# Kernel optimization log

Hardware: AMD Instinct MI355X
Metric: run time of the kernel (lower is better)

## Reference

```python
import jax, jax.numpy as jnp
import numpy as np

N, E, B, T = 50000, 800000, 256, 50
IN_DIM, H, C1, C2, Q_DIM, LH = 128, 4, 32, 128, 32, 128
EPS = 1e-5


def setup_inputs() -> dict:
    key = jax.random.key(0)
    ks = jax.random.split(key, 24)
    g = 0.05
    inp = {
        'x': jax.random.normal(ks[0], (N, IN_DIM), jnp.float32),
        'edge_index': jax.random.randint(ks[1], (2, E), 0, N, jnp.int32),
        'batch': jnp.sort(jax.random.randint(ks[2], (N,), 0, B, jnp.int32)),
        'quant': jax.random.normal(ks[3], (B, T, Q_DIM), jnp.float32),
        # GATConv(128 -> 32, heads=4, concat)
        'gat_W': jax.random.normal(ks[4], (IN_DIM, H * C1), jnp.float32) * g,
        'gat_att_src': jax.random.normal(ks[5], (H, C1), jnp.float32) * g,
        'gat_att_dst': jax.random.normal(ks[6], (H, C1), jnp.float32) * g,
        'gat_b': jnp.zeros((H * C1,), jnp.float32),
        # BN1 over 128 channels (eval mode)
        'bn1_gamma': jnp.ones((H * C1,), jnp.float32),
        'bn1_beta': jnp.zeros((H * C1,), jnp.float32),
        'bn1_mean': jax.random.normal(ks[7], (H * C1,), jnp.float32) * 0.01,
        'bn1_var': jnp.ones((H * C1,), jnp.float32),
        # GCNConv(128 -> 128)
        'gcn_W': jax.random.normal(ks[8], (H * C1, C2), jnp.float32) * g,
        'gcn_b': jnp.zeros((C2,), jnp.float32),
        'bn2_gamma': jnp.ones((C2,), jnp.float32),
        'bn2_beta': jnp.zeros((C2,), jnp.float32),
        'bn2_mean': jax.random.normal(ks[9], (C2,), jnp.float32) * 0.01,
        'bn2_var': jnp.ones((C2,), jnp.float32),
        # GlobalAttention gate: Linear(C2 -> 1)
        'gate_W': jax.random.normal(ks[10], (1, C2), jnp.float32) * g,
        'gate_b': jnp.zeros((1,), jnp.float32),
        # LSTM(Q_DIM -> LH), torch gate order i,f,g,o
        'lstm_Wih': jax.random.normal(ks[11], (4 * LH, Q_DIM), jnp.float32) * g,
        'lstm_Whh': jax.random.normal(ks[12], (4 * LH, LH), jnp.float32) * g,
        'lstm_bih': jnp.zeros((4 * LH,), jnp.float32),
        'lstm_bhh': jnp.zeros((4 * LH,), jnp.float32),
        # final Linear(C2+LH -> 1)
        'fc_W': jax.random.normal(ks[13], (1, C2 + LH), jnp.float32) * g,
        'fc_b': jnp.zeros((1,), jnp.float32),
    }
    return inp


def _segment_softmax(e, seg, num_segments):
    m = jax.ops.segment_max(e, seg, num_segments=num_segments)
    ex = jnp.exp(e - m[seg])
    s = jax.ops.segment_sum(ex, seg, num_segments=num_segments)
    return ex / (s[seg] + 1e-16)


def _bn_eval(x, gamma, beta, mean, var):
    return gamma * (x - mean) * jax.lax.rsqrt(var + EPS) + beta


def _forward(x, edge_index, batch, quant,
             gat_W, gat_att_src, gat_att_dst, gat_b,
             bn1_gamma, bn1_beta, bn1_mean, bn1_var,
             gcn_W, gcn_b, bn2_gamma, bn2_beta, bn2_mean, bn2_var,
             gate_W, gate_b,
             lstm_Wih, lstm_Whh, lstm_bih, lstm_bhh,
             fc_W, fc_b):
    n = x.shape[0]
    loops = jnp.arange(n, dtype=edge_index.dtype)
    ei = jnp.concatenate([edge_index, jnp.stack([loops, loops])], axis=1)  # add self loops
    src, dst = ei[0], ei[1]

    # ---- GATConv ----
    xw = (x @ gat_W).reshape(n, H, C1)                      # [N,H,C1]
    a_src = jnp.sum(xw * gat_att_src, axis=-1)              # [N,H]
    a_dst = jnp.sum(xw * gat_att_dst, axis=-1)
    e = jax.nn.leaky_relu(a_src[src] + a_dst[dst], 0.2)     # [E+N,H]
    alpha = _segment_softmax(e, dst, n)                     # softmax over in-edges per dst
    msg = xw[src] * alpha[:, :, None]                       # [E+N,H,C1]
    h = jax.ops.segment_sum(msg, dst, num_segments=n).reshape(n, H * C1) + gat_b

    h = jax.nn.elu(h)
    h = _bn_eval(h, bn1_gamma, bn1_beta, bn1_mean, bn1_var)

    # ---- GCNConv (sym-normalized with self loops) ----
    deg = jax.ops.segment_sum(jnp.ones_like(dst, jnp.float32), dst, num_segments=n)
    dinv = jnp.where(deg > 0, jax.lax.rsqrt(deg), 0.0)
    norm = dinv[src] * dinv[dst]                            # [E+N]
    hw = h @ gcn_W                                          # [N,C2]
    h2 = jax.ops.segment_sum(hw[src] * norm[:, None], dst, num_segments=n) + gcn_b

    h2 = jax.nn.elu(h2)
    h2 = _bn_eval(h2, bn2_gamma, bn2_beta, bn2_mean, bn2_var)

    # ---- GlobalAttention pooling over graphs ----
    gate = (h2 @ gate_W.T + gate_b)[:, 0]                   # [N]
    score = _segment_softmax(gate, batch, B)
    graph_rep = jax.ops.segment_sum(score[:, None] * h2, batch, num_segments=B)  # [B,C2]

    # ---- LSTM over quant series ----
    def step(carry, xt):
        hh, cc = carry
        gates = xt @ lstm_Wih.T + hh @ lstm_Whh.T + lstm_bih + lstm_bhh
        i, f, gg, o = jnp.split(gates, 4, axis=-1)
        cc = jax.nn.sigmoid(f) * cc + jax.nn.sigmoid(i) * jnp.tanh(gg)
        hh = jax.nn.sigmoid(o) * jnp.tanh(cc)
        return (hh, cc), None

    h0 = jnp.zeros((B, LH), quant.dtype)
    (hT, _), _ = jax.lax.scan(step, (h0, h0), jnp.swapaxes(quant, 0, 1))

    combined = jnp.concatenate([graph_rep, hT], axis=1)     # [B, C2+LH]
    out = (combined @ fc_W.T + fc_b)[:, 0]                  # [B]
    return out


def reference(x, edge_index, batch, quant,
              gat_W, gat_att_src, gat_att_dst, gat_b,
              bn1_gamma, bn1_beta, bn1_mean, bn1_var,
              gcn_W, gcn_b, bn2_gamma, bn2_beta, bn2_mean, bn2_var,
              gate_W, gate_b,
              lstm_Wih, lstm_Whh, lstm_bih, lstm_bhh,
              fc_W, fc_b):
    return _forward(x, edge_index, batch, quant,
                    gat_W, gat_att_src, gat_att_dst, gat_b,
                    bn1_gamma, bn1_beta, bn1_mean, bn1_var,
                    gcn_W, gcn_b, bn2_gamma, bn2_beta, bn2_mean, bn2_var,
                    gate_W, gate_b,
                    lstm_Wih, lstm_Whh, lstm_bih, lstm_bhh,
                    fc_W, fc_b)
```

## Files before the change

kernel.cpp:

```cpp
#include <hip/hip_runtime.h>
#include <cfloat>
#include <cstddef>

constexpr int KIN   = 128;
constexpr int KQD   = 32;
constexpr int KT    = 50;
constexpr int KLH   = 128;
constexpr float BN_EPS = 1e-5f;

typedef __attribute__((ext_vector_type(8))) short bf16x8;
typedef __attribute__((ext_vector_type(4))) float f32x4;
union U8 { bf16x8 v; unsigned u[4]; };

__device__ __forceinline__ float elu_f(float x)  { return x > 0.f ? x : (__expf(x) - 1.f); }
__device__ __forceinline__ float leaky_f(float x){ return x > 0.f ? x : 0.2f * x; }

__device__ __forceinline__ unsigned bfpack(float lo, float hi) {
    unsigned ul = __float_as_uint(lo), uh = __float_as_uint(hi);
    ul += 0x7FFFu + ((ul >> 16) & 1u);
    uh += 0x7FFFu + ((uh >> 16) & 1u);
    return (ul >> 16) | (uh & 0xFFFF0000u);
}
__device__ __forceinline__ unsigned short bf1(float v) {
    unsigned u = __float_as_uint(v);
    u += 0x7FFFu + ((u >> 16) & 1u);
    return (unsigned short)(u >> 16);
}
__device__ __forceinline__ float bflo(unsigned u) { return __uint_as_float(u << 16); }
__device__ __forceinline__ float bfhi(unsigned u) { return __uint_as_float(u & 0xFFFF0000u); }

__device__ __forceinline__ bf16x8 pack8(float4 p, float4 q) {
    U8 t;
    t.u[0] = bfpack(p.x, p.y); t.u[1] = bfpack(p.z, p.w);
    t.u[2] = bfpack(q.x, q.y); t.u[3] = bfpack(q.z, q.w);
    return t.v;
}

__global__ void k_deg(const int* __restrict__ ei, int E, int* __restrict__ deg) {
    int e = blockIdx.x * blockDim.x + threadIdx.x;
    if (e < E) atomicAdd(&deg[ei[E + e]], 1);
}

__global__ __launch_bounds__(1024)
void k_scan_a(const int* __restrict__ deg, int n, int* __restrict__ bsum) {
    __shared__ int wsum[16];
    int tid = threadIdx.x, lane = tid & 63, w = tid >> 6;
    int i0 = blockIdx.x * 4096 + tid * 4;
    int t = 0;
    #pragma unroll
    for (int j = 0; j < 4; j++) t += (i0 + j < n) ? deg[i0 + j] : 0;
    #pragma unroll
    for (int d = 1; d < 64; d <<= 1) t += __shfl_xor(t, d);
    if (lane == 0) wsum[w] = t;
    __syncthreads();
    if (tid == 0) {
        int s = 0;
        #pragma unroll
        for (int k = 0; k < 16; k++) s += wsum[k];
        bsum[blockIdx.x] = s;
    }
}

__global__ void k_scan_b(int* __restrict__ bsum, int nb) {
    if (threadIdx.x == 0) {
        int run = 0;
        for (int i = 0; i < nb; i++) { int v = bsum[i]; bsum[i] = run; run += v; }
    }
}

__global__ __launch_bounds__(1024)
void k_scan_c(const int* __restrict__ deg, int n, const int* __restrict__ bsum,
              int* __restrict__ offsets, int* __restrict__ cursor,
              float* __restrict__ dinv) {
    __shared__ int wsum[16];
    int tid = threadIdx.x, lane = tid & 63, w = tid >> 6;
    int i0 = blockIdx.x * 4096 + tid * 4;
    int v[4];
    #pragma unroll
    for (int j = 0; j < 4; j++) v[j] = (i0 + j < n) ? deg[i0 + j] : 0;
    int tsum = v[0] + v[1] + v[2] + v[3];
    int sc = tsum;
    #pragma unroll
    for (int d = 1; d < 64; d <<= 1) {
        int o = __shfl_up(sc, d);
        if (lane >= d) sc += o;
    }
    if (lane == 63) wsum[w] = sc;
    __syncthreads();
    if (w == 0) {
        int xx = (lane < 16) ? wsum[lane] : 0;
        #pragma unroll
        for (int d = 1; d < 16; d <<= 1) {
            int o = __shfl_up(xx, d);
            if (lane >= d) xx += o;
        }
        if (lane < 16) wsum[lane] = xx;
    }
    __syncthreads();
    int run = bsum[blockIdx.x] + ((w > 0) ? wsum[w - 1] : 0) + sc - tsum;
    #pragma unroll
    for (int j = 0; j < 4; j++) {
        int i = i0 + j;
        if (i < n) {
            cursor[i]      = run;
            offsets[i + 1] = run + v[j];
            dinv[i]        = rsqrtf((float)(v[j] + 1));
            run += v[j];
        }
    }
    if (blockIdx.x == 0 && tid == 0) offsets[0] = 0;
}

__global__ void k_fill(const int* __restrict__ ei, int E, int* __restrict__ cursor,
                       int* __restrict__ csr_src) {
    int e = blockIdx.x * blockDim.x + threadIdx.x;
    if (e < E) {
        int s = ei[e], d = ei[E + e];
        int pos = atomicAdd(&cursor[d], 1);
        csr_src[pos] = s;
    }
}

template <bool ATT>
__global__ __launch_bounds__(256, 4)
void k_gemm_mfma(const float* __restrict__ X, const float* __restrict__ W,
                 unsigned* __restrict__ Yb, int nrows,
                 const float* __restrict__ attS, const float* __restrict__ attD,
                 float* __restrict__ a_src, float* __restrict__ a_dst) {
    __shared__ float tile[16][132];
    __shared__ float as_sh[128], ad_sh[128];
    int tid  = threadIdx.x;
    int lane = tid & 63;
    int wv   = tid >> 6;
    if (ATT && tid < 128) { as_sh[tid] = attS[tid]; ad_sh[tid] = attD[tid]; }
    int l16 = lane & 15;
    int kq  = (lane >> 4) * 8;
    bf16x8 bfr[2][4];
    #pragma unroll
    for (int nt = 0; nt < 2; nt++) {
        int n = wv * 32 + nt * 16 + l16;
        #pragma unroll
        for (int kk = 0; kk < 4; kk++) {
            int k0 = kk * 32 + kq;
            float f[8];
            #pragma unroll
            for (int j = 0; j < 8; j++) f[j] = W[(size_t)(k0 + j) * 128 + n];
            U8 t;
            t.u[0] = bfpack(f[0], f[1]); t.u[1] = bfpack(f[2], f[3]);
            t.u[2] = bfpack(f[4], f[5]); t.u[3] = bfpack(f[6], f[7]);
            bfr[nt][kk] = t.v;
        }
    }
    int nch = (nrows + 15) / 16;
    for (int ch = blockIdx.x; ch < nch; ch += gridDim.x) {
        int r0 = ch * 16;
        int r  = r0 + l16;
        bool rok = r < nrows;
        const float* xr = X + (size_t)r * 128 + kq;
        float4 z4 = make_float4(0.f, 0.f, 0.f, 0.f);
        bf16x8 afr[4];
        #pragma unroll
        for (int kk = 0; kk < 4; kk++) {
            float4 p = rok ? *reinterpret_cast<const float4*>(xr + kk * 32)     : z4;
            float4 q = rok ? *reinterpret_cast<const float4*>(xr + kk * 32 + 4) : z4;
            afr[kk] = pack8(p, q);
        }
        f32x4 acc0 = {0.f, 0.f, 0.f, 0.f};
        f32x4 acc1 = {0.f, 0.f, 0.f, 0.f};
        #pragma unroll
        for (int kk = 0; kk < 4; kk++) {
            acc0 = __builtin_amdgcn_mfma_f32_16x16x32_bf16(afr[kk], bfr[0][kk], acc0, 0, 0, 0);
            acc1 = __builtin_amdgcn_mfma_f32_16x16x32_bf16(afr[kk], bfr[1][kk], acc1, 0, 0, 0);
        }
        __syncthreads();
        int rowb = (lane >> 4) * 4;
        int cb   = wv * 32 + l16;
        #pragma unroll
        for (int reg = 0; reg < 4; reg++) {
            tile[rowb + reg][cb]      = acc0[reg];
            tile[rowb + reg][cb + 16] = acc1[reg];
        }
        __syncthreads();
        #pragma unroll
        for (int i = 0; i < 4; i++) {
            int idx = tid + i * 256;
            int row = idx >> 6, cp = idx & 63;
            int rr = r0 + row;
            if (rr < nrows) {
                float2 f = *reinterpret_cast<const float2*>(&tile[row][cp * 2]);
                Yb[(size_t)rr * 64 + cp] = bfpack(f.x, f.y);
            }
        }
        if (ATT && tid < 64) {
            int rr2 = tid >> 2, h = tid & 3;
            if (r0 + rr2 < nrows) {
                float ps = 0.f, pd = 0.f;
                #pragma unroll
                for (int j = 0; j < 32; j++) {
                    float v = tile[rr2][h * 32 + j];
                    ps += v * as_sh[h * 32 + j];
                    pd += v * ad_sh[h * 32 + j];
                }
                a_src[(size_t)(r0 + rr2) * 4 + h] = ps;
                a_dst[(size_t)(r0 + rr2) * 4 + h] = pd;
            }
        }
    }
}

__global__ __launch_bounds__(256)
void k_gat_agg(const int* __restrict__ offsets, const int* __restrict__ csr_src,
               const float* __restrict__ a_src, const float* __restrict__ a_dst,
               const unsigned* __restrict__ xwb, const float* __restrict__ bias,
               const float* __restrict__ g1, const float* __restrict__ b1,
               const float* __restrict__ mu1, const float* __restrict__ var1,
               float* __restrict__ hout, int n) {
    __shared__ int   src_sh[4][64];
    __shared__ float al_sh[4][4][64];
    int lane = threadIdx.x & 63;
    int wv   = threadIdx.x >> 6;
    int wid  = (blockIdx.x * blockDim.x + threadIdx.x) >> 6;
    int nw   = (gridDim.x * blockDim.x) >> 6;
    int hP   = lane >> 4;
    int c0 = lane * 2, c1 = c0 + 1;
    float bi0 = bias[c0], bi1 = bias[c1];
    float A0 = g1[c0] * rsqrtf(var1[c0] + BN_EPS);
    float A1 = g1[c1] * rsqrtf(var1[c1] + BN_EPS);
    float B0 = b1[c0] - mu1[c0] * A0;
    float B1 = b1[c1] - mu1[c1] * A1;
    for (int node = wid; node < n; node += nw) {
        int beg = offsets[node], end = offsets[node + 1];
        int rowlen = end - beg, total = rowlen + 1;
        float4 adv = *reinterpret_cast<const float4*>(&a_dst[(size_t)node * 4]);
        int sv = (lane < rowlen) ? csr_src[beg + lane] : node;
        float4 as4 = *reinterpret_cast<const float4*>(&a_src[(size_t)sv * 4]);
        float e0 = leaky_f(as4.x + adv.x), e1 = leaky_f(as4.y + adv.y);
        float e2 = leaky_f(as4.z + adv.z), e3 = leaky_f(as4.w + adv.w);
        float m[4] = {-FLT_MAX, -FLT_MAX, -FLT_MAX, -FLT_MAX};
        if (lane < total) { m[0] = e0; m[1] = e1; m[2] = e2; m[3] = e3; }
        for (int i = lane + 64; i < total; i += 64) {
            int src = (i < rowlen) ? csr_src[beg + i] : node;
            float4 a4 = *reinterpret_cast<const float4*>(&a_src[(size_t)src * 4]);
            m[0] = fmaxf(m[0], leaky_f(a4.x + adv.x));
            m[1] = fmaxf(m[1], leaky_f(a4.y + adv.y));
            m[2] = fmaxf(m[2], leaky_f(a4.z + adv.z));
            m[3] = fmaxf(m[3], leaky_f(a4.w + adv.w));
        }
        #pragma unroll
        for (int off = 32; off; off >>= 1) {
            #pragma unroll
            for (int h = 0; h < 4; h++) m[h] = fmaxf(m[h], __shfl_xor(m[h], off));
        }
        float ex[4] = {0.f, 0.f, 0.f, 0.f};
        if (lane < total) {
            ex[0] = __expf(e0 - m[0]); ex[1] = __expf(e1 - m[1]);
            ex[2] = __expf(e2 - m[2]); ex[3] = __expf(e3 - m[3]);
        }
        float s[4] = {ex[0], ex[1], ex[2], ex[3]};
        for (int i = lane + 64; i < total; i += 64) {
            int src = (i < rowlen) ? csr_src[beg + i] : node;
            float4 a4 = *reinterpret_cast<const float4*>(&a_src[(size_t)src * 4]);
            s[0] += __expf(leaky_f(a4.x + adv.x) - m[0]);
            s[1] += __expf(leaky_f(a4.y + adv.y) - m[1]);
            s[2] += __expf(leaky_f(a4.z + adv.z) - m[2]);
            s[3] += __expf(leaky_f(a4.w + adv.w) - m[3]);
        }
        #pragma unroll
        for (int off = 32; off; off >>= 1) {
            #pragma unroll
            for (int h = 0; h < 4; h++) s[h] += __shfl_xor(s[h], off);
        }
        float inv[4];
        #pragma unroll
        for (int h = 0; h < 4; h++) inv[h] = 1.f / (s[h] + 1e-16f);
        src_sh[wv][lane] = sv;
        #pragma unroll
        for (int h = 0; h < 4; h++) al_sh[wv][h][lane] = ex[h] * inv[h];
        __builtin_amdgcn_wave_barrier();
        float acc0 = 0.f, acc1 = 0.f;
        int cnt = min(total, 64);
        {
            int i = 0;
            for (; i + 8 <= cnt; i += 8) {
                int   sj[8]; float aj[8]; unsigned uj[8];
                #pragma unroll
                for (int q = 0; q < 8; q++) { sj[q] = src_sh[wv][i + q]; aj[q] = al_sh[wv][hP][i + q]; }
                #pragma unroll
                for (int q = 0; q < 8; q++) uj[q] = xwb[(size_t)sj[q] * 64 + lane];
                #pragma unroll
                for (int q = 0; q < 8; q++) { acc0 += aj[q] * bflo(uj[q]); acc1 += aj[q] * bfhi(uj[q]); }
            }
            for (; i < cnt; i++) {
                int src  = src_sh[wv][i];
                float aP = al_sh[wv][hP][i];
                unsigned u = xwb[(size_t)src * 64 + lane];
                acc0 += aP * bflo(u);
                acc1 += aP * bfhi(u);
            }
        }
        for (int base = 64; base < total; base += 64) {
            __builtin_amdgcn_wave_barrier();
            int i = base + lane;
            int src2 = node;
            float a0v = 0.f, a1v = 0.f, a2v = 0.f, a3v = 0.f;
            if (i < total) {
                if (i < rowlen) src2 = csr_src[beg + i];
                float4 a4 = *reinterpret_cast<const float4*>(&a_src[(size_t)src2 * 4]);
                a0v = __expf(leaky_f(a4.x + adv.x) - m[0]) * inv[0];
                a1v = __expf(leaky_f(a4.y + adv.y) - m[1]) * inv[1];
                a2v = __expf(leaky_f(a4.z + adv.z) - m[2]) * inv[2];
                a3v = __expf(leaky_f(a4.w + adv.w) - m[3]) * inv[3];
            }
            src_sh[wv][lane] = src2;
            al_sh[wv][0][lane] = a0v; al_sh[wv][1][lane] = a1v;
            al_sh[wv][2][lane] = a2v; al_sh[wv][3][lane] = a3v;
            __builtin_amdgcn_wave_barrier();
            int cnt2 = min(total - base, 64);
            for (int j = 0; j < cnt2; j++) {
                int src  = src_sh[wv][j];
                float aP = al_sh[wv][hP][j];
                unsigned u = xwb[(size_t)src * 64 + lane];
                acc0 += aP * bflo(u);
                acc1 += aP * bfhi(u);
            }
        }
        __builtin_amdgcn_wave_barrier();
        float vA = elu_f(acc0 + bi0);
        float vB = elu_f(acc1 + bi1);
        vA = vA * A0 + B0;
        vB = vB * A1 + B1;
        *reinterpret_cast<float2*>(&hout[(size_t)node * 128 + c0]) =
            make_float2(vA, vB);
    }
}

__global__ __launch_bounds__(256)
void k_gcn_agg(const int* __restrict__ offsets, const int* __restrict__ csr_src,
               const float* __restrict__ dinv, const unsigned* __restrict__ hwb,
               const float* __restrict__ bias,
               const float* __restrict__ g2, const float* __restrict__ b2,
               const float* __restrict__ mu2, const float* __restrict__ var2,
               const float* __restrict__ gateW, const float* __restrict__ gateB,
               float* __restrict__ h2, float* __restrict__ gate, int n) {
    __shared__ int   src_sh[4][64];
    __shared__ float w_sh[4][64];
    int lane = threadIdx.x & 63;
    int wv   = threadIdx.x >> 6;
    int wid  = (blockIdx.x * blockDim.x + threadIdx.x) >> 6;
    int nw   = (gridDim.x * blockDim.x) >> 6;
    int c0 = lane * 2, c1 = c0 + 1;
    float bi0 = bias[c0], bi1 = bias[c1];
    float A0 = g2[c0] * rsqrtf(var2[c0] + BN_EPS);
    float A1 = g2[c1] * rsqrtf(var2[c1] + BN_EPS);
    float B0 = b2[c0] - mu2[c0] * A0;
    float B1 = b2[c1] - mu2[c1] * A1;
    float gw0 = gateW[c0], gw1 = gateW[c1], gB = gateB[0];
    for (int node = wid; node < n; node += nw) {
        int beg = offsets[node], end = offsets[node + 1];
        int rowlen = end - beg;
        float dn = dinv[node];
        unsigned us = hwb[(size_t)node * 64 + lane];
        float acc0 = dn * dn * bflo(us);
        float acc1 = dn * dn * bfhi(us);
        for (int base = 0; base < rowlen; base += 64) {
            __builtin_amdgcn_wave_barrier();
            int i = base + lane;
            int src2 = node;
            float wv2 = 0.f;
            if (i < rowlen) { src2 = csr_src[beg + i]; wv2 = dinv[src2] * dn; }
            src_sh[wv][lane] = src2;
            w_sh[wv][lane]   = wv2;
            __builtin_amdgcn_wave_barrier();
            int cnt = min(rowlen - base, 64);
            int j = 0;
            for (; j + 8 <= cnt; j += 8) {
                int   sj[8]; float wj[8]; unsigned uj[8];
                #pragma unroll
                for (int q = 0; q < 8; q++) { sj[q] = src_sh[wv][j + q]; wj[q] = w_sh[wv][j + q]; }
                #pragma unroll
                for (int q = 0; q < 8; q++) uj[q] = hwb[(size_t)sj[q] * 64 + lane];
                #pragma unroll
                for (int q = 0; q < 8; q++) { acc0 += wj[q] * bflo(uj[q]); acc1 += wj[q] * bfhi(uj[q]); }
            }
            for (; j < cnt; j++) {
                int src = src_sh[wv][j];
                float w = w_sh[wv][j];
                unsigned u = hwb[(size_t)src * 64 + lane];
                acc0 += w * bflo(u);
                acc1 += w * bfhi(u);
            }
        }
        __builtin_amdgcn_wave_barrier();
        float vA = elu_f(acc0 + bi0);
        float vB = elu_f(acc1 + bi1);
        vA = vA * A0 + B0;
        vB = vB * A1 + B1;
        *reinterpret_cast<float2*>(&h2[(size_t)node * 128 + c0]) =
            make_float2(vA, vB);
        float p = vA * gw0 + vB * gw1;
        #pragma unroll
        for (int off = 32; off; off >>= 1) p += __shfl_xor(p, off);
        if (lane == 0) gate[node] = p + gB;
    }
}

__device__ __forceinline__ int lbound(const int* a, int n, int key) {
    int lo = 0, hi = n;
    while (lo < hi) { int mid = (lo + hi) >> 1; if (a[mid] < key) lo = mid + 1; else hi = mid; }
    return lo;
}

__global__ __launch_bounds__(256)
void k_pool(const int* __restrict__ batch, const float* __restrict__ gate,
            const float* __restrict__ h2, const float* __restrict__ hT,
            const float* __restrict__ fcW, const float* __restrict__ fcB,
            float* __restrict__ out, int n) {
    int b = blockIdx.x, tid = threadIdx.x;
    __shared__ float red[256];
    __shared__ float sc_sh[256];
    int start = lbound(batch, n, b);
    int end   = lbound(batch, n, b + 1);
    float m = -FLT_MAX;
    for (int i = start + tid; i < end; i += 256) m = fmaxf(m, gate[i]);
    red[tid] = m; __syncthreads();
    for (int s2 = 128; s2 > 0; s2 >>= 1) {
        if (tid < s2) red[tid] = fmaxf(red[tid], red[tid + s2]);
        __syncthreads();
    }
    m = red[0]; __syncthreads();
    float s = 0.f;
    for (int i = start + tid; i < end; i += 256) s += __expf(gate[i] - m);
    red[tid] = s; __syncthreads();
    for (int s2 = 128; s2 > 0; s2 >>= 1) {
        if (tid < s2) red[tid] += red[tid + s2];
        __syncthreads();
    }
    float inv = 1.f / (red[0] + 1e-16f);
    __syncthreads();
    int j = tid & 127, half = tid >> 7;
    float acc = 0.f;
    for (int base = start; base < end; base += 256) {
        int cnt = min(256, end - base);
        __syncthreads();
        if (tid < cnt) sc_sh[tid] = __expf(gate[base + tid] - m) * inv;
        __syncthreads();
        for (int ii = half; ii < cnt; ii += 2)
            acc += sc_sh[ii] * h2[(size_t)(base + ii) * 128 + j];
    }
    red[tid] = acc; __syncthreads();
    if (half == 0) sc_sh[j] = red[j] + red[128 + j];
    __syncthreads();
    float p = 0.f;
    if (tid < 128)
        p = fcW[tid] * sc_sh[tid] + fcW[128 + tid] * hT[(size_t)b * 128 + tid];
    red[tid] = p; __syncthreads();
    for (int s2 = 128; s2 > 0; s2 >>= 1) {
        if (tid < s2) red[tid] += red[tid + s2];
        __syncthreads();
    }
    if (tid == 0) out[b] = red[0] + fcB[0];
}

__global__ __launch_bounds__(256)
void k_xproj(const float* __restrict__ quant, const float* __restrict__ Wih,
             const float* __restrict__ bih, const float* __restrict__ bhh,
             float* __restrict__ xproj) {
    int blk = blockIdx.x;
    int chunk = blk / KT, s = blk % KT;
    int lane = threadIdx.x & 63, w = threadIdx.x >> 6;
    int l15 = lane & 15, kq8 = (lane >> 4) * 8;
    int b = chunk * 16 + l15;
    const float* xr = &quant[(size_t)b * (KT * KQD) + s * KQD + kq8];
    bf16x8 ax = pack8(*reinterpret_cast<const float4*>(xr),
                      *reinterpret_cast<const float4*>(xr + 4));
    #pragma unroll
    for (int ti = 0; ti < 8; ti++) {
        int tc = w * 8 + ti;
        int gcol = w * 128 + ti * 16 + l15;
        const float* wr = &Wih[(size_t)gcol * KQD + kq8];
        bf16x8 bw = pack8(*reinterpret_cast<const float4*>(wr),
                          *reinterpret_cast<const float4*>(wr + 4));
        f32x4 acc = {0.f, 0.f, 0.f, 0.f};
        acc = __builtin_amdgcn_mfma_f32_16x16x32_bf16(ax, bw, acc, 0, 0, 0);
        float bv = bih[gcol] + bhh[gcol];
        acc[0] += bv; acc[1] += bv; acc[2] += bv; acc[3] += bv;
        *reinterpret_cast<f32x4*>(
            &xproj[(((size_t)chunk * KT + s) * 32 + tc) * 256 + lane * 4]) = acc;
    }
}

__global__ __launch_bounds__(512)
void k_lstm2(const float* __restrict__ xproj, const float* __restrict__ Whh,
             float* __restrict__ hstate) {
    __shared__ unsigned short h16[2][16][148];
    int t = threadIdx.x, lane = t & 63, w = t >> 6;
    int chunk = blockIdx.x;
    int l15 = lane & 15, kq8 = (lane >> 4) * 8;
    int j = w * 16 + l15;
    int rowq = (lane >> 4) * 4;
    bf16x8 whh_f[4][4];
    #pragma unroll
    for (int c = 0; c < 4; c++) {
        int col = c * 128 + j;
        #pragma unroll
        for (int kk = 0; kk < 4; kk++) {
            const float* wr = &Whh[(size_t)col * 128 + kk * 32 + kq8];
            whh_f[c][kk] = pack8(*reinterpret_cast<const float4*>(wr),
                                 *reinterpret_cast<const float4*>(wr + 4));
        }
    }
    for (int p = t; p < 16 * 148; p += 512) {
        int r = p / 148, cc = p - r * 148;
        h16[0][r][cc] = 0;
    }
    float cst[4] = {0.f, 0.f, 0.f, 0.f};
    const float* xb = xproj + ((size_t)chunk * KT) * 32 * 256;
    f32x4 xgA = *reinterpret_cast<const f32x4*>(&xb[(0 * 8 + w) * 256 + lane * 4]);
    f32x4 xgB = *reinterpret_cast<const f32x4*>(&xb[(1 * 8 + w) * 256 + lane * 4]);
    f32x4 xgC = *reinterpret_cast<const f32x4*>(&xb[(2 * 8 + w) * 256 + lane * 4]);
    f32x4 xgD = *reinterpret_cast<const f32x4*>(&xb[(3 * 8 + w) * 256 + lane * 4]);
    int cur = 0;
    __syncthreads();
    for (int s = 0; s < KT; s++) {
        f32x4 nA, nB, nC, nD;
        if (s + 1 < KT) {
            const float* xs = &xb[((size_t)(s + 1) * 32 + w) * 256 + lane * 4];
            nA = *reinterpret_cast<const f32x4*>(&xs[0 * 8 * 256]);
            nB = *reinterpret_cast<const f32x4*>(&xs[1 * 8 * 256]);
            nC = *reinterpret_cast<const f32x4*>(&xs[2 * 8 * 256]);
            nD = *reinterpret_cast<const f32x4*>(&xs[3 * 8 * 256]);
        }
        f32x4 ai = xgA, af = xgB, ag = xgC, ao = xgD;
        #pragma unroll
        for (int kk = 0; kk < 4; kk++) {
            bf16x8 ah = *reinterpret_cast<const bf16x8*>(&h16[cur][l15][kk * 32 + kq8]);
            ai = __builtin_amdgcn_mfma_f32_16x16x32_bf16(ah, whh_f[0][kk], ai, 0, 0, 0);
            af = __builtin_amdgcn_mfma_f32_16x16x32_bf16(ah, whh_f[1][kk], af, 0, 0, 0);
            ag = __builtin_amdgcn_mfma_f32_16x16x32_bf16(ah, whh_f[2][kk], ag, 0, 0, 0);
            ao = __builtin_amdgcn_mfma_f32_16x16x32_bf16(ah, whh_f[3][kk], ao, 0, 0, 0);
        }
        int nxt = cur ^ 1;
        #pragma unroll
        for (int r = 0; r < 4; r++) {
            float eiv = __expf(fminf(-ai[r], 25.f));
            float efv = __expf(fminf(-af[r], 25.f));
            float egv = __expf(fminf(2.f * ag[r], 50.f));
            float eov = __expf(fminf(-ao[r], 25.f));
            float pi = 1.f + eiv, pf = 1.f + efv;
            float gp = egv + 1.f, gm = egv - 1.f;
            float P  = pi * gp;
            float D  = pf * P;
            float cn = fmaf(cst[r], P, gm * pf) * __builtin_amdgcn_rcpf(D);
            cst[r] = cn;
            float ecv = __expf(fminf(2.f * cn, 50.f));
            float D2  = (1.f + eov) * (ecv + 1.f);
            float hv  = (ecv - 1.f) * __builtin_amdgcn_rcpf(D2);
            h16[nxt][rowq + r][j] = bf1(hv);
        }
        xgA = nA; xgB = nB; xgC = nC; xgD = nD;
        __syncthreads();
        cur = nxt;
    }
    int b0 = chunk * 16;
    for (int p = t; p < 16 * KLH; p += 512) {
        int row = p >> 7, jj = p & 127;
        hstate[(size_t)(b0 + row) * KLH + jj] =
            __uint_as_float((unsigned)h16[cur][row][jj] << 16);
    }
}

extern "C" void kernel_launch(void* const* d_in, const int* in_sizes, int n_in,
                              void* d_out, int out_size, void* d_ws, size_t ws_size,
                              hipStream_t stream) {
    const float* x     = (const float*)d_in[0];
    const int*   ei    = (const int*)  d_in[1];
    const int*   batch = (const int*)  d_in[2];
    const float* quant = (const float*)d_in[3];
    const float* gatW  = (const float*)d_in[4];
    const float* attS  = (const float*)d_in[5];
    const float* attD  = (const float*)d_in[6];
    const float* gatB  = (const float*)d_in[7];
    const float* bn1g  = (const float*)d_in[8];
    const float* bn1b  = (const float*)d_in[9];
    const float* bn1m  = (const float*)d_in[10];
    const float* bn1v  = (const float*)d_in[11];
    const float* gcnW  = (const float*)d_in[12];
    const float* gcnB  = (const float*)d_in[13];
    const float* bn2g  = (const float*)d_in[14];
    const float* bn2b  = (const float*)d_in[15];
    const float* bn2m  = (const float*)d_in[16];
    const float* bn2v  = (const float*)d_in[17];
    const float* gateW = (const float*)d_in[18];
    const float* gateB = (const float*)d_in[19];
    const float* Wih   = (const float*)d_in[20];
    const float* Whh   = (const float*)d_in[21];
    const float* bih   = (const float*)d_in[22];
    const float* bhh   = (const float*)d_in[23];
    const float* fcW   = (const float*)d_in[24];
    const float* fcB   = (const float*)d_in[25];

    int N = in_sizes[0] / KIN;
    int E = in_sizes[1] / 2;
    int B = in_sizes[3] / (KT * KQD);
    int nchunks = B / 16;

    char* ws = (char*)d_ws;
    size_t off = 0;
    auto alloc = [&](size_t bytes) -> void* {
        void* p = ws + off;
        off += (bytes + 511) & ~(size_t)511;
        return p;
    };
    int nb = (N + 4095) / 4096;
    int*      deg     = (int*)     alloc((size_t)N * 4);
    int*      offsets = (int*)     alloc((size_t)(N + 1) * 4);
    int*      cursor  = (int*)     alloc((size_t)N * 4);
    float*    dinv    = (float*)   alloc((size_t)N * 4);
    int*      csr_src = (int*)     alloc((size_t)E * 4);
    int*      bsum    = (int*)     alloc((size_t)nb * 4);
    float*    a_src   = (float*)   alloc((size_t)N * 16);
    float*    a_dst   = (float*)   alloc((size_t)N * 16);
    unsigned* xwb     = (unsigned*)alloc((size_t)N * 256);
    float*    hbuf    = (float*)   alloc((size_t)N * 512);
    float*    gate    = (float*)   alloc((size_t)N * 4);
    float*    hstate  = (float*)   alloc((size_t)B * KLH * 4);
    float*    xproj   = (float*)   alloc((size_t)nchunks * KT * 32 * 256 * 4);

    hipMemsetAsync(deg, 0, (size_t)N * 4, stream);
    int eb = (E + 255) / 256;
    k_deg   <<<eb, 256, 0, stream>>>(ei, E, deg);
    k_scan_a<<<nb, 1024, 0, stream>>>(deg, N, bsum);
    k_scan_b<<<1, 64, 0, stream>>>(bsum, nb);
    k_scan_c<<<nb, 1024, 0, stream>>>(deg, N, bsum, offsets, cursor, dinv);
    k_fill  <<<eb, 256, 0, stream>>>(ei, E, cursor, csr_src);

    k_xproj<<<nchunks * KT, 256, 0, stream>>>(quant, Wih, bih, bhh, xproj);
    k_lstm2<<<nchunks, 512, 0, stream>>>(xproj, Whh, hstate);

    k_gemm_mfma<true ><<<1024, 256, 0, stream>>>(x, gatW, xwb, N, attS, attD, a_src, a_dst);
    k_gat_agg<<<3072, 256, 0, stream>>>(offsets, csr_src, a_src, a_dst, xwb, gatB,
                                        bn1g, bn1b, bn1m, bn1v, hbuf, N);
    k_gemm_mfma<false><<<1024, 256, 0, stream>>>(hbuf, gcnW, xwb, N,
                                                 nullptr, nullptr, nullptr, nullptr);
    k_gcn_agg<<<3072, 256, 0, stream>>>(offsets, csr_src, dinv, xwb, gcnB,
                                        bn2g, bn2b, bn2m, bn2v, gateW, gateB,
                                        hbuf, gate, N);
    k_pool<<<B, 256, 0, stream>>>(batch, gate, hbuf, hstate, fcW, fcB,
                                  (float*)d_out, N);
}
```

Measured before the change: 409.4 us.

## Merge LSTM recurrence, GAT projection GEMM and CSR fill into one launch

Combines three independent stages (the serial LSTM recurrence over 16 chunk blocks, the attention-projection GEMM and the CSR edge fill) into one kernel whose blocks branch on block index. The long, low-occupancy LSTM blocks come first so the GEMM and fill blocks can run alongside them instead of waiting in separate launches. Shared memory becomes a union of the two layouts. The GEMM is rewritten for 512-thread blocks with one 16-row chunk per iteration, and the 512-thread launch bound may change register pressure and occupancy for the GEMM and fill paths.

```diff
diff --git a/kernel.cpp b/kernel.cpp
--- a/kernel.cpp
+++ b/kernel.cpp
@@ -109,16 +109,6 @@
         }
     }
     if (blockIdx.x == 0 && tid == 0) offsets[0] = 0;
-}
-
-__global__ void k_fill(const int* __restrict__ ei, int E, int* __restrict__ cursor,
-                       int* __restrict__ csr_src) {
-    int e = blockIdx.x * blockDim.x + threadIdx.x;
-    if (e < E) {
-        int s = ei[e], d = ei[E + e];
-        int pos = atomicAdd(&cursor[d], 1);
-        csr_src[pos] = s;
-    }
 }
 
 template <bool ATT>
@@ -489,13 +479,104 @@
     }
 }
 
+struct GemmSh { float tile[16][132]; float as[128]; float ad[128]; };
+struct LstmSh { unsigned short h16[2][16][148]; };
+union  FusedSh { GemmSh g; LstmSh l; };
+
 __global__ __launch_bounds__(512)
-void k_lstm2(const float* __restrict__ xproj, const float* __restrict__ Whh,
-             float* __restrict__ hstate) {
-    __shared__ unsigned short h16[2][16][148];
+void k_fused(
+             const float* __restrict__ xproj, const float* __restrict__ Whh,
+             float* __restrict__ hstate, int nchunks,
+             const float* __restrict__ X, const float* __restrict__ W,
+             unsigned* __restrict__ Yb, int nrows,
+             const float* __restrict__ attS, const float* __restrict__ attD,
+             float* __restrict__ a_src, float* __restrict__ a_dst, int ngemm,
+             const int* __restrict__ ei, int E, int* __restrict__ cursor,
+             int* __restrict__ csr_src) {
+    __shared__ FusedSh sh;
+    int bid = (int)blockIdx.x;
     int t = threadIdx.x, lane = t & 63, w = t >> 6;
-    int chunk = blockIdx.x;
+
+    if (bid >= nchunks + ngemm) {
+        int e = (bid - nchunks - ngemm) * 512 + t;
+        if (e < E) {
+            int s = ei[e], d = ei[E + e];
+            int pos = atomicAdd(&cursor[d], 1);
+            csr_src[pos] = s;
+        }
+        return;
+    }
+
     int l15 = lane & 15, kq8 = (lane >> 4) * 8;
+
+    if (bid >= nchunks) {
+        if (t < 128) { sh.g.as[t] = attS[t]; sh.g.ad[t] = attD[t]; }
+        int n = w * 16 + l15;
+        bf16x8 bfr[4];
+        #pragma unroll
+        for (int kk = 0; kk < 4; kk++) {
+            int k0 = kk * 32 + kq8;
+            float f[8];
+            #pragma unroll
+            for (int jj = 0; jj < 8; jj++) f[jj] = W[(size_t)(k0 + jj) * 128 + n];
+            U8 tp;
+            tp.u[0] = bfpack(f[0], f[1]); tp.u[1] = bfpack(f[2], f[3]);
+            tp.u[2] = bfpack(f[4], f[5]); tp.u[3] = bfpack(f[6], f[7]);
+            bfr[kk] = tp.v;
+        }
+        int nch = (nrows + 15) / 16;
+        for (int ch = bid - nchunks; ch < nch; ch += ngemm) {
+            int r0 = ch * 16;
+            int r  = r0 + l15;
+            bool rok = r < nrows;
+            const float* xr = X + (size_t)r * 128 + kq8;
+            float4 z4 = make_float4(0.f, 0.f, 0.f, 0.f);
+            bf16x8 afr[4];
+            #pragma unroll
+            for (int kk = 0; kk < 4; kk++) {
+                float4 p = rok ? *reinterpret_cast<const float4*>(xr + kk * 32)     : z4;
+                float4 q = rok ? *reinterpret_cast<const float4*>(xr + kk * 32 + 4) : z4;
+                afr[kk] = pack8(p, q);
+            }
+            f32x4 acc = {0.f, 0.f, 0.f, 0.f};
+            #pragma unroll
+            for (int kk = 0; kk < 4; kk++)
+                acc = __builtin_amdgcn_mfma_f32_16x16x32_bf16(afr[kk], bfr[kk], acc, 0, 0, 0);
+            __syncthreads();
+            int rowb = (lane >> 4) * 4;
+            #pragma unroll
+            for (int reg = 0; reg < 4; reg++)
+                sh.g.tile[rowb + reg][n] = acc[reg];
+            __syncthreads();
+            #pragma unroll
+            for (int i = 0; i < 2; i++) {
+                int idx = t + i * 512;
+                int row = idx >> 6, cp = idx & 63;
+                int rr = r0 + row;
+                if (rr < nrows) {
+                    float2 f = *reinterpret_cast<const float2*>(&sh.g.tile[row][cp * 2]);
+                    Yb[(size_t)rr * 64 + cp] = bfpack(f.x, f.y);
+                }
+            }
+            if (t < 64) {
+                int rr2 = t >> 2, h = t & 3;
+                if (r0 + rr2 < nrows) {
+                    float ps = 0.f, pd = 0.f;
+                    #pragma unroll
+                    for (int jj = 0; jj < 32; jj++) {
+                        float v = sh.g.tile[rr2][h * 32 + jj];
+                        ps += v * sh.g.as[h * 32 + jj];
+                        pd += v * sh.g.ad[h * 32 + jj];
+                    }
+                    a_src[(size_t)(r0 + rr2) * 4 + h] = ps;
+                    a_dst[(size_t)(r0 + rr2) * 4 + h] = pd;
+                }
+            }
+        }
+        return;
+    }
+
+    int chunk = bid;
     int j = w * 16 + l15;
     int rowq = (lane >> 4) * 4;
     bf16x8 whh_f[4][4];
@@ -511,7 +592,7 @@
     }
     for (int p = t; p < 16 * 148; p += 512) {
         int r = p / 148, cc = p - r * 148;
-        h16[0][r][cc] = 0;
+        sh.l.h16[0][r][cc] = 0;
     }
     float cst[4] = {0.f, 0.f, 0.f, 0.f};
     const float* xb = xproj + ((size_t)chunk * KT) * 32 * 256;
@@ -533,7 +614,7 @@
         f32x4 ai = xgA, af = xgB, ag = xgC, ao = xgD;
         #pragma unroll
         for (int kk = 0; kk < 4; kk++) {
-            bf16x8 ah = *reinterpret_cast<const bf16x8*>(&h16[cur][l15][kk * 32 + kq8]);
+            bf16x8 ah = *reinterpret_cast<const bf16x8*>(&sh.l.h16[cur][l15][kk * 32 + kq8]);
             ai = __builtin_amdgcn_mfma_f32_16x16x32_bf16(ah, whh_f[0][kk], ai, 0, 0, 0);
             af = __builtin_amdgcn_mfma_f32_16x16x32_bf16(ah, whh_f[1][kk], af, 0, 0, 0);
             ag = __builtin_amdgcn_mfma_f32_16x16x32_bf16(ah, whh_f[2][kk], ag, 0, 0, 0);
@@ -555,7 +636,7 @@
             float ecv = __expf(fminf(2.f * cn, 50.f));
             float D2  = (1.f + eov) * (ecv + 1.f);
             float hv  = (ecv - 1.f) * __builtin_amdgcn_rcpf(D2);
-            h16[nxt][rowq + r][j] = bf1(hv);
+            sh.l.h16[nxt][rowq + r][j] = bf1(hv);
         }
         xgA = nA; xgB = nB; xgC = nC; xgD = nD;
         __syncthreads();
@@ -565,7 +646,7 @@
     for (int p = t; p < 16 * KLH; p += 512) {
         int row = p >> 7, jj = p & 127;
         hstate[(size_t)(b0 + row) * KLH + jj] =
-            __uint_as_float((unsigned)h16[cur][row][jj] << 16);
+            __uint_as_float((unsigned)sh.l.h16[cur][row][jj] << 16);
     }
 }
 
@@ -632,12 +713,16 @@
     k_scan_a<<<nb, 1024, 0, stream>>>(deg, N, bsum);
     k_scan_b<<<1, 64, 0, stream>>>(bsum, nb);
     k_scan_c<<<nb, 1024, 0, stream>>>(deg, N, bsum, offsets, cursor, dinv);
-    k_fill  <<<eb, 256, 0, stream>>>(ei, E, cursor, csr_src);
 
     k_xproj<<<nchunks * KT, 256, 0, stream>>>(quant, Wih, bih, bhh, xproj);
-    k_lstm2<<<nchunks, 512, 0, stream>>>(xproj, Whh, hstate);
-
-    k_gemm_mfma<true ><<<1024, 256, 0, stream>>>(x, gatW, xwb, N, attS, attD, a_src, a_dst);
+
+    int ngemm = 1024;
+    int nfill = (E + 511) / 512;
+    k_fused<<<nchunks + ngemm + nfill, 512, 0, stream>>>(
+        xproj, Whh, hstate, nchunks,
+        x, gatW, xwb, N, attS, attD, a_src, a_dst, ngemm,
+        ei, E, cursor, csr_src);
+
     k_gat_agg<<<3072, 256, 0, stream>>>(offsets, csr_src, a_src, a_dst, xwb, gatB,
                                         bn1g, bn1b, bn1m, bn1v, hbuf, N);
     k_gemm_mfma<false><<<1024, 256, 0, stream>>>(hbuf, gcnW, xwb, N,
```

New measurement: 385.3 us. 5.9% less time.
